# Kernel optimization log

Hardware: AMD Instinct MI355X
Metric: run time of the kernel (lower is better)

The kernel has to match this reference:

```python
import jax, jax.numpy as jnp
import numpy as np

BN_EPS = 1e-5
ITER_N = 5

def _bn(x, gamma, beta, mean, var, axis):
    shape = [1] * x.ndim
    shape[axis] = -1
    r = lambda v: v.reshape(shape)
    return (x - r(mean)) * (r(gamma) / jnp.sqrt(r(var) + BN_EPS)) + r(beta)

def _covpool(x):
    # x: (B, d, M); MPNCOV CovpoolLayer: y = x @ I_hat @ x^T, I_hat = (1/M)I - (1/M^2)11^T
    M = x.shape[-1]
    I_hat = (-1.0 / (M * M)) * jnp.ones((M, M), x.dtype) + (1.0 / M) * jnp.eye(M, dtype=x.dtype)
    return jnp.einsum('bdm,mn,ben->bde', x, I_hat, x)

def _sqrtm_ns(A, iterN=ITER_N):
    # MPNCOV SqrtmLayer: trace-normalized Newton-Schulz iteration
    d = A.shape[-1]
    I3 = 3.0 * jnp.eye(d, dtype=A.dtype)
    normA = jnp.trace(A, axis1=1, axis2=2) / 3.0          # (B,)
    A_n = A / normA[:, None, None]
    ZY = 0.5 * (I3 - A_n)
    Y = A_n @ ZY
    Z = ZY
    for _ in range(iterN - 2):
        ZY = 0.5 * (I3 - Z @ Y)
        Y = Y @ ZY
        Z = ZY @ Z
    YZY = 0.5 * (Y @ (I3 - Z @ Y))
    return YZY * jnp.sqrt(normA)[:, None, None]

def setup_inputs() -> dict:
    key = jax.random.key(0)
    ks = jax.random.split(key, 12)
    B, C, H, W = 64, 1024, 16, 16
    D, R = 128, H * W  # att_dim, sp_reso
    return {
        'x': jax.random.normal(ks[0], (B, C, H, W), jnp.float32),
        'w_dr': jax.random.normal(ks[1], (D, C), jnp.float32) * 0.02,
        'b_dr': jax.random.normal(ks[2], (D,), jnp.float32) * 0.02,
        'bn1_gamma': jnp.ones((D,), jnp.float32),
        'bn1_beta': jnp.zeros((D,), jnp.float32),
        'bn1_mean': jax.random.normal(ks[3], (D,), jnp.float32) * 0.1,
        'bn1_var': jax.random.uniform(ks[4], (D,), jnp.float32, 0.5, 1.5),
        'bn2_gamma': jnp.ones((R,), jnp.float32),
        'bn2_beta': jnp.zeros((R,), jnp.float32),
        'bn2_mean': jax.random.normal(ks[5], (R,), jnp.float32) * 0.1,
        'bn2_var': jax.random.uniform(ks[6], (R,), jnp.float32, 0.5, 1.5),
        'rc_w': jax.random.normal(ks[7], (R,), jnp.float32) * 0.1 + 1.0,
        'rc_b': jax.random.normal(ks[8], (R,), jnp.float32) * 0.02,
        'fc_w': jax.random.normal(ks[9], (R, R * R), jnp.float32) * 0.004,
        'fc_b': jax.random.normal(ks[10], (R,), jnp.float32) * 0.02,
    }

def reference(x, w_dr, b_dr, bn1_gamma, bn1_beta, bn1_mean, bn1_var,
              bn2_gamma, bn2_beta, bn2_mean, bn2_var, rc_w, rc_b, fc_w, fc_b):
    B, C, H, W = x.shape
    # 1x1 dimension-reduction conv + BN + ReLU
    y = jnp.einsum('bchw,dc->bdhw', x, w_dr) + b_dr[None, :, None, None]
    y = jax.nn.relu(_bn(y, bn1_gamma, bn1_beta, bn1_mean, bn1_var, axis=1))
    # (B, D, HW) -> (B, HW, D): HW spatial positions as 'channels', D as samples
    y = y.reshape(B, -1, H * W).transpose(0, 2, 1)
    cov = _covpool(y)                  # (B, HW, HW)
    s = _sqrtm_ns(cov, ITER_N)         # (B, HW, HW)
    # row BN over first HW axis (channels of the (B, HW, HW, 1) view)
    s = _bn(s, bn2_gamma, bn2_beta, bn2_mean, bn2_var, axis=1)
    # grouped (depthwise) 1x1 row conv: per-row scale + bias
    s = s * rc_w[None, :, None] + rc_b[None, :, None]
    att = jax.nn.sigmoid(s.reshape(B, -1) @ fc_w.T + fc_b)   # (B, HW)
    att = att.reshape(B, 1, H, W)
    return x * att
```

## Files before the change

kernel.cpp:

```cpp
#include <hip/hip_runtime.h>

typedef unsigned short u16;
typedef unsigned int   u32;
typedef __attribute__((ext_vector_type(8))) short bf8;
typedef __attribute__((ext_vector_type(4))) float f4;
typedef __attribute__((ext_vector_type(16))) float f16f;

#define MFMA(a,b,c)   __builtin_amdgcn_mfma_f32_16x16x32_bf16(a,b,c,0,0,0)
#define MFMA32(a,b,c) __builtin_amdgcn_mfma_f32_32x32x16_bf16(a,b,c,0,0,0)

__device__ __forceinline__ u16 f2bf(float f){
  u32 u = __float_as_uint(f);
  u += 0x7fffu + ((u >> 16) & 1u);
  return (u16)(u >> 16);
}
__device__ __forceinline__ float bf2f(u16 h){ return __uint_as_float(((u32)h) << 16); }
__device__ __forceinline__ u32 pk2(float a, float b){ return (u32)f2bf(a) | ((u32)f2bf(b) << 16); }

__device__ __forceinline__ void glds16(const u16* g, u16* l){
  __builtin_amdgcn_global_load_lds((const __attribute__((address_space(1))) u32*)g,
                                   (__attribute__((address_space(3))) u32*)l, 16, 0, 0);
}

__device__ __forceinline__ bf8 ldsFrag(const char* m, int row0, int k0, int pitch){
  int l = threadIdx.x & 63;
  int r = row0 + (l & 15);
  int kb = ((k0 + ((l >> 4) << 3)) << 1) ^ ((r & 7) << 4);
  return *(const bf8*)(m + r * pitch + kb);
}
__device__ __forceinline__ void ldsPut(char* m, int row, int col, int pitch, u16 v){
  int kb = (col << 1) ^ ((row & 7) << 4);
  *(u16*)(m + row * pitch + kb) = v;
}

__device__ __forceinline__ bf8 fragNS(const char* m, int r0, int ks, int l){
  int r = r0 + (l & 31);
  int kb = ((ks << 5) + ((l >> 5) << 4)) ^ ((r & 15) << 4);
  return *(const bf8*)(m + r * 256 + kb);
}
__device__ __forceinline__ bf8 fragWT(const char* m, int r0, int ks, int l){
  int r = r0 + (l & 31);
  int kb = ((ks << 5) + ((l >> 5) << 4)) ^ ((r & 15) << 4);
  return *(const bf8*)(m + r * 512 + kb);
}
__device__ __forceinline__ char* nsAddr(char* m, int row, int col4){
  return m + row * 256 + ((col4 << 1) ^ ((row & 15) << 4));
}

__device__ __forceinline__ void mmPass(const char* A, const char* B, f16f (&acc)[2][2],
                                       int R0, int C0, int l){
  #pragma unroll
  for (int ks = 0; ks < 8; ++ks){
    bf8 a0 = fragNS(A, R0,      ks, l);
    bf8 a1 = fragNS(A, R0 + 32, ks, l);
    bf8 b0 = fragNS(B, C0,      ks, l);
    bf8 b1 = fragNS(B, C0 + 32, ks, l);
    acc[0][0] = MFMA32(a0, b0, acc[0][0]); acc[0][1] = MFMA32(a0, b1, acc[0][1]);
    acc[1][0] = MFMA32(a1, b0, acc[1][0]); acc[1][1] = MFMA32(a1, b1, acc[1][1]);
  }
}

__device__ __forceinline__ void writeTile(char* D, const f16f (&acc)[2][2], int R0, int C0, int l,
                                          float scale, float dval, const uint2* adv){
  #pragma unroll
  for (int ri = 0; ri < 2; ++ri)
  #pragma unroll
  for (int ci = 0; ci < 2; ++ci)
  #pragma unroll
  for (int g = 0; g < 4; ++g){
    int srow = C0 + ci * 32 + (l & 31);
    int scol = R0 + ri * 32 + g * 8 + ((l >> 5) << 2);
    float v[4];
    #pragma unroll
    for (int q = 0; q < 4; ++q){
      float x = scale * acc[ri][ci][g * 4 + q];
      x += ((scol + q) == srow) ? dval : 0.f;
      v[q] = x;
    }
    if (adv){
      uint2 ad = adv[(ri * 2 + ci) * 4 + g];
      v[0] += 1.5f * bf2f((u16)ad.x);
      v[1] += 1.5f * bf2f((u16)(ad.x >> 16));
      v[2] += 1.5f * bf2f((u16)ad.y);
      v[3] += 1.5f * bf2f((u16)(ad.y >> 16));
    }
    *(uint2*)nsAddr(D, srow, scol) = make_uint2(pk2(v[0], v[1]), pk2(v[2], v[3]));
  }
}

__global__ __launch_bounds__(256) void k_prep(const float* __restrict__ wdr,
                                              float* __restrict__ logits,
                                              u16* __restrict__ prep){
  int i = blockIdx.x * 256 + threadIdx.x;
  if (i < 16384) logits[i] = 0.f;
  #pragma unroll
  for (int j = 0; j < 2; ++j){
    int e = i + j * 65536;
    int chunk = e >> 13, rem = e & 8191, d = rem >> 6, cb2 = rem & 63;
    int c = ((cb2 * 2) ^ ((d & 7) << 4)) >> 1;
    prep[e] = f2bf(wdr[d * 1024 + chunk * 64 + c]);
  }
}

__global__ __launch_bounds__(512) void k_conv(
    const u16* __restrict__ wprep, const float* __restrict__ x, const float* __restrict__ bdr,
    const float* __restrict__ g1, const float* __restrict__ be1,
    const float* __restrict__ m1, const float* __restrict__ v1,
    u16* __restrict__ Wg, u16* __restrict__ WTg){
  __shared__ union {
    struct { u16 A[4][8192]; u16 Bt[2][2048]; } s;
    struct { float y[128 * 33]; float musum[512]; float mu[32]; } e;
  } sm;
  int t = threadIdx.x;
  int b = blockIdx.x >> 3, hw0 = (blockIdx.x & 7) * 32;
  const float* xb = x + (size_t)b * 262144 + hw0;

  int w = t >> 6, l = t & 63;
  int d0 = (w >> 1) * 32, hh = (w & 1) * 16;
  int lc = l & 15, lr = (l >> 4) * 4;

  const f4 fz = {0.f, 0.f, 0.f, 0.f};
  f4 acc[2]; acc[0] = fz; acc[1] = fz;

  int cp = t >> 5, hwl = t & 31;
  int bo0 = (4 * cp) ^ ((hwl & 7) << 4);
  int bo1 = (4 * cp + 64) ^ ((hwl & 7) << 4);

  float br[3][4];
  #pragma unroll
  for (int j = 0; j < 3; ++j){
    glds16(wprep + j * 8192 + t * 8,        sm.s.A[j] + t * 8);
    glds16(wprep + j * 8192 + 4096 + t * 8, sm.s.A[j] + 4096 + t * 8);
    __builtin_amdgcn_sched_barrier(0);
    int c0 = j * 64;
    br[j][0] = xb[(size_t)(c0 + 2 * cp)      * 256 + hwl];
    br[j][1] = xb[(size_t)(c0 + 2 * cp + 1)  * 256 + hwl];
    br[j][2] = xb[(size_t)(c0 + 2 * cp + 32) * 256 + hwl];
    br[j][3] = xb[(size_t)(c0 + 2 * cp + 33) * 256 + hwl];
    __builtin_amdgcn_sched_barrier(0);
  }

  #pragma unroll
  for (int k = 0; k < 16; ++k){
    if (k <= 12){
      const u16* src = wprep + (k + 3) * 8192;
      glds16(src + t * 8,        sm.s.A[(k + 3) & 3] + t * 8);
      glds16(src + 4096 + t * 8, sm.s.A[(k + 3) & 3] + 4096 + t * 8);
    }
    __builtin_amdgcn_sched_barrier(0);
    if (k <= 12)      asm volatile("s_waitcnt vmcnt(14)" ::: "memory");
    else if (k == 13) asm volatile("s_waitcnt vmcnt(12)" ::: "memory");
    else if (k == 14) asm volatile("s_waitcnt vmcnt(6)" ::: "memory");
    else              asm volatile("s_waitcnt vmcnt(0)" ::: "memory");
    __builtin_amdgcn_sched_barrier(0);
    *(u32*)((char*)sm.s.Bt[k & 1] + hwl * 128 + bo0) = pk2(br[k % 3][0], br[k % 3][1]);
    *(u32*)((char*)sm.s.Bt[k & 1] + hwl * 128 + bo1) = pk2(br[k % 3][2], br[k % 3][3]);
    __builtin_amdgcn_sched_barrier(0);
    if (k <= 12){
      int c0 = (k + 3) * 64;
      br[k % 3][0] = xb[(size_t)(c0 + 2 * cp)      * 256 + hwl];
      br[k % 3][1] = xb[(size_t)(c0 + 2 * cp + 1)  * 256 + hwl];
      br[k % 3][2] = xb[(size_t)(c0 + 2 * cp + 32) * 256 + hwl];
      br[k % 3][3] = xb[(size_t)(c0 + 2 * cp + 33) * 256 + hwl];
    }
    __builtin_amdgcn_sched_barrier(0);
    asm volatile("s_waitcnt lgkmcnt(0)" ::: "memory");
    __builtin_amdgcn_sched_barrier(0);
    __builtin_amdgcn_s_barrier();
    __builtin_amdgcn_sched_barrier(0);
    #pragma unroll
    for (int ks = 0; ks < 2; ++ks){
      int k0 = ks * 32;
      bf8 a0 = ldsFrag((const char*)sm.s.A[k & 3], d0,      k0, 128);
      bf8 a1 = ldsFrag((const char*)sm.s.A[k & 3], d0 + 16, k0, 128);
      bf8 b0 = ldsFrag((const char*)sm.s.Bt[k & 1], hh, k0, 128);
      acc[0] = MFMA(a0, b0, acc[0]);
      acc[1] = MFMA(a1, b0, acc[1]);
    }
    __builtin_amdgcn_sched_barrier(0);
    __builtin_amdgcn_s_barrier();
    __builtin_amdgcn_sched_barrier(0);
  }
  __syncthreads();

  #pragma unroll
  for (int i = 0; i < 2; ++i)
    #pragma unroll
    for (int r = 0; r < 4; ++r){
      int d = d0 + i * 16 + lr + r;
      float s1 = g1[d] * rsqrtf(v1[d] + 1e-5f);
      float t1 = (bdr[d] - m1[d]) * s1 + be1[d];
      int hwp = hh + lc;
      sm.e.y[d * 33 + hwp] = fmaxf(acc[i][r] * s1 + t1, 0.f);
    }
  __syncthreads();
  { int part = t >> 5, col = t & 31;
    float s = 0.f;
    #pragma unroll
    for (int i2 = 0; i2 < 8; ++i2) s += sm.e.y[(part * 8 + i2) * 33 + col];
    sm.e.musum[part * 32 + col] = s;
  }
  __syncthreads();
  if (t < 32){
    float m = 0.f;
    #pragma unroll
    for (int p = 0; p < 16; ++p) m += sm.e.musum[p * 32 + t];
    sm.e.mu[t] = m * (1.0f / 128.0f);
  }
  __syncthreads();
  const float ISM = 0.08838834764831845f;
  { int hwp = t >> 4, dc = (t & 15) * 8;
    float muv = sm.e.mu[hwp];
    u32 q[4];
    #pragma unroll
    for (int jj = 0; jj < 4; ++jj){
      float a = (sm.e.y[(dc + 2 * jj)     * 33 + hwp] - muv) * ISM;
      float c = (sm.e.y[(dc + 2 * jj + 1) * 33 + hwp] - muv) * ISM;
      q[jj] = pk2(a, c);
    }
    *(uint4*)(Wg + ((size_t)(b * 256 + hw0 + hwp) * 128 + dc)) = make_uint4(q[0], q[1], q[2], q[3]);
  }
  { int d = t >> 2, hc = (t & 3) * 8;
    u32 q[4];
    #pragma unroll
    for (int jj = 0; jj < 4; ++jj){
      int h0 = hc + 2 * jj, h1 = hc + 2 * jj + 1;
      float a = (sm.e.y[d * 33 + h0] - sm.e.mu[h0]) * ISM;
      float c = (sm.e.y[d * 33 + h1] - sm.e.mu[h1]) * ISM;
      q[jj] = pk2(a, c);
    }
    *(uint4*)(WTg + ((size_t)(b * 128 + d) * 256 + hw0 + hc)) = make_uint4(q[0], q[1], q[2], q[3]);
  }
}

extern __shared__ char smns[];
__global__ __launch_bounds__(512, 2) void k_ns(const u16* __restrict__ WT,
                                               u16* __restrict__ yf, float* __restrict__ normAg){
  int b = blockIdx.x, t = threadIdx.x;
  char* Yb = smns;
  char* Zb = smns + 32768;
  char* T1 = smns + 65536;
  char* T2 = smns + 98304;
  char* T3 = smns + 131072;
  char* WTl = smns + 65536;
  char* G   = T3;
  float* trp = (float*)smns;

  int w = t >> 6, l = t & 63;
  int wq = w & 3;
  int R0 = (wq >> 1) * 64, C0 = (wq & 1) * 64;

  { const u16* src = WT + (size_t)b * 32768;
    int row = t >> 2, q = t & 3;
    #pragma unroll
    for (int j = 0; j < 8; ++j) {
      int c16 = q + j * 4;
      bf8 v = *(const bf8*)(src + row * 256 + c16 * 8);
      int ph = c16 ^ (row & 15);
      *(bf8*)(WTl + row * 512 + ph * 16) = v;
    }
  }
  if (t == 0) *trp = 0.f;
  __syncthreads();

  int R0g = (w & 3) * 32, C0g = (w >> 2) * 64;
  const f16f fz16 = {};
  f16f gac[2]; gac[0] = fz16; gac[1] = fz16;
  #pragma unroll
  for (int ks = 0; ks < 16; ++ks){
    bf8 a  = fragWT(WTl, R0g,      ks, l);
    bf8 b0 = fragWT(WTl, C0g,      ks, l);
    bf8 b1 = fragWT(WTl, C0g + 32, ks, l);
    gac[0] = MFMA32(a, b0, gac[0]);
    gac[1] = MFMA32(a, b1, gac[1]);
  }
  float tp = 0.f;
  #pragma unroll
  for (int ci = 0; ci < 2; ++ci)
    #pragma unroll
    for (int e = 0; e < 16; ++e){
      int row = R0g + (e & 3) + 8 * (e >> 2) + ((l >> 5) << 2);
      int col = C0g + ci * 32 + (l & 31);
      if (row == col) tp += gac[ci][e];
    }
  #pragma unroll
  for (int off = 32; off > 0; off >>= 1) tp += __shfl_down(tp, off);
  if (l == 0) atomicAdd(trp, tp);
  __syncthreads();

  float normA = fmaxf(*trp / 3.0f, 1e-12f);
  if (t == 0) normAg[b] = normA;
  float inv = 1.0f / normA;
  #pragma unroll
  for (int ci = 0; ci < 2; ++ci)
    #pragma unroll
    for (int g = 0; g < 4; ++g){
      int srow = C0g + ci * 32 + (l & 31);
      int scol = R0g + g * 8 + ((l >> 5) << 2);
      float v0 = gac[ci][g * 4 + 0] * inv, v1 = gac[ci][g * 4 + 1] * inv;
      float v2 = gac[ci][g * 4 + 2] * inv, v3 = gac[ci][g * 4 + 3] * inv;
      *(uint2*)nsAddr(G, srow, scol) = make_uint2(pk2(v0, v1), pk2(v2, v3));
    }
  __syncthreads();

  bf8 gA[8], gB[8];
  #pragma unroll
  for (int ks = 0; ks < 8; ++ks){
    gA[ks] = fragNS(G, C0,      ks, l);
    gB[ks] = fragNS(G, C0 + 32, ks, l);
  }
  { int row = t >> 2, q4 = t & 3;
    #pragma unroll
    for (int j = 0; j < 4; ++j){
      int c16 = q4 * 4 + j;
      int ph = c16 ^ (row & 15);
      bf8 gg = *(const bf8*)(G + row * 256 + ph * 16);
      bf8 yv, zv;
      #pragma unroll
      for (int e = 0; e < 8; ++e){
        int col = c16 * 8 + e;
        float y = -0.5f * bf2f((u16)gg[e]) + ((col == row) ? 1.5f : 0.f);
        yv[e] = (short)f2bf(y);
        zv[e] = (col == row) ? (short)f2bf(-0.5f) : (short)0;
      }
      *(bf8*)(Yb + row * 256 + ph * 16) = yv;
      *(bf8*)(Zb + row * 256 + ph * 16) = zv;
    }
  }
  __syncthreads();

  float z0 = 1.5f;
  for (int it = 0; it < 4; ++it){
    {
      f16f acc[2][2]; acc[0][0] = fz16; acc[0][1] = fz16; acc[1][0] = fz16; acc[1][1] = fz16;
      const char* As = (w < 4) ? Zb : Yb;
      #pragma unroll
      for (int ks = 0; ks < 8; ++ks){
        bf8 a0 = fragNS(As, R0,      ks, l);
        bf8 a1 = fragNS(As, R0 + 32, ks, l);
        acc[0][0] = MFMA32(a0, gA[ks], acc[0][0]); acc[0][1] = MFMA32(a0, gB[ks], acc[0][1]);
        acc[1][0] = MFMA32(a1, gA[ks], acc[1][0]); acc[1][1] = MFMA32(a1, gB[ks], acc[1][1]);
      }
      writeTile((w < 4) ? T1 : T3, acc, R0, C0, l, 1.0f, (w < 4) ? z0 : 0.f, nullptr);
    }
    __syncthreads();

    uint2 adv[16];
    {
      const char* addsrc = (w < 4) ? Zb : Yb;
      #pragma unroll
      for (int ri = 0; ri < 2; ++ri)
      #pragma unroll
      for (int ci = 0; ci < 2; ++ci)
      #pragma unroll
      for (int g = 0; g < 4; ++g){
        int srow = C0 + ci * 32 + (l & 31);
        int scol = R0 + ri * 32 + g * 8 + ((l >> 5) << 2);
        adv[(ri * 2 + ci) * 4 + g] = *(const uint2*)nsAddr((char*)addsrc, srow, scol);
      }
      int hC0 = C0 + ((w >> 2) << 5);
      f16f a2[2]; a2[0] = fz16; a2[1] = fz16;
      #pragma unroll
      for (int ks = 0; ks < 8; ++ks){
        bf8 a0 = fragNS(T1, R0,      ks, l);
        bf8 a1 = fragNS(T1, R0 + 32, ks, l);
        bf8 b0 = fragNS(Yb, hC0,     ks, l);
        a2[0] = MFMA32(a0, b0, a2[0]);
        a2[1] = MFMA32(a1, b0, a2[1]);
      }
      #pragma unroll
      for (int ri = 0; ri < 2; ++ri)
      #pragma unroll
      for (int g = 0; g < 4; ++g){
        int srow = hC0 + (l & 31);
        int scol = R0 + ri * 32 + g * 8 + ((l >> 5) << 2);
        float v0 = -0.5f * a2[ri][g * 4 + 0], v1 = -0.5f * a2[ri][g * 4 + 1];
        float v2 = -0.5f * a2[ri][g * 4 + 2], v3 = -0.5f * a2[ri][g * 4 + 3];
        *(uint2*)nsAddr(T2, srow, scol) = make_uint2(pk2(v0, v1), pk2(v2, v3));
      }
    }
    __syncthreads();

    if ((w >= 4) || (it < 3)){
      f16f acc[2][2]; acc[0][0] = fz16; acc[0][1] = fz16; acc[1][0] = fz16; acc[1][1] = fz16;
      const char* A3 = (w < 4) ? T2 : T3;
      const char* B3 = (w < 4) ? T1 : T2;
      mmPass(A3, B3, acc, R0, C0, l);
      writeTile((w < 4) ? Zb : Yb, acc, R0, C0, l, 1.0f, 0.f, adv);
    }
    __syncthreads();
    z0 *= 1.5f;
  }

  { int row = t >> 2, q = t & 3;
    u16* dst = yf + (size_t)b * 16384 + row * 128;
    #pragma unroll
    for (int j = 0; j < 4; ++j) {
      int c16 = q * 4 + j;
      int ph = c16 ^ (row & 15);
      *(bf8*)(dst + c16 * 8) = *(const bf8*)(Yb + row * 256 + ph * 16);
    }
  }
}

extern __shared__ char smex[];
__global__ __launch_bounds__(512) void k_expand(
    const u16* __restrict__ Wg, const u16* __restrict__ yf, const float* __restrict__ normAg,
    const float* __restrict__ g2, const float* __restrict__ be2, const float* __restrict__ m2,
    const float* __restrict__ v2, const float* __restrict__ rcw, const float* __restrict__ rcb,
    u16* __restrict__ sp){
  int blk = blockIdx.x, b = blk >> 2, iband = blk & 3;
  char* Bm = smex;
  char* Yl = smex + 65536;
  char* El = smex + 98304;
  int t = threadIdx.x;
  { const u16* src = Wg + (size_t)b * 32768;
    int row = t >> 1, q = t & 1;
    #pragma unroll
    for (int j = 0; j < 8; ++j) {
      int c16 = q + j * 2;
      bf8 v = *(const bf8*)(src + row * 128 + c16 * 8);
      int ph = c16 ^ (row & 7);
      *(bf8*)(Bm + row * 256 + ph * 16) = v;
    } }
  { const u16* src = yf + (size_t)b * 16384;
    int row = t >> 2, q = t & 3;
    #pragma unroll
    for (int j = 0; j < 4; ++j) {
      int c16 = q + j * 4;
      bf8 v = *(const bf8*)(src + row * 128 + c16 * 8);
      int ph = c16 ^ (row & 7);
      *(bf8*)(Yl + row * 256 + ph * 16) = v;
    } }
  __syncthreads();
  int w = t >> 6, l = t & 63, lc = l & 15, lr = (l >> 4) * 4;
  const f4 fz = {0.f, 0.f, 0.f, 0.f};
  { int r0 = (w >> 2) * 32, c0 = (w & 3) * 32;
    f4 acc[2][2];
    acc[0][0] = fz; acc[0][1] = fz; acc[1][0] = fz; acc[1][1] = fz;
    #pragma unroll
    for (int kk = 0; kk < 4; ++kk) {
      int k0 = kk * 32;
      bf8 a0 = ldsFrag(Bm, iband * 64 + r0,      k0, 256);
      bf8 a1 = ldsFrag(Bm, iband * 64 + r0 + 16, k0, 256);
      bf8 b0 = ldsFrag(Yl, c0,      k0, 256);
      bf8 b1 = ldsFrag(Yl, c0 + 16, k0, 256);
      acc[0][0] = MFMA(a0, b0, acc[0][0]); acc[0][1] = MFMA(a0, b1, acc[0][1]);
      acc[1][0] = MFMA(a1, b0, acc[1][0]); acc[1][1] = MFMA(a1, b1, acc[1][1]);
    }
    #pragma unroll
    for (int i = 0; i < 2; ++i)
      #pragma unroll
      for (int j = 0; j < 2; ++j)
        #pragma unroll
        for (int r = 0; r < 4; ++r)
          ldsPut(El, r0 + i * 16 + lr + r, c0 + j * 16 + lc, 256, f2bf(acc[i][j][r]));
  }
  __syncthreads();
  { float invs = rsqrtf(normAg[b]);
    int r0 = (w >> 2) * 32, c0 = (w & 3) * 64;
    f4 acc[2][4];
    #pragma unroll
    for (int i = 0; i < 2; ++i)
      #pragma unroll
      for (int j = 0; j < 4; ++j) acc[i][j] = fz;
    #pragma unroll
    for (int kk = 0; kk < 4; ++kk) {
      int k0 = kk * 32;
      bf8 a0 = ldsFrag(El, r0,      k0, 256);
      bf8 a1 = ldsFrag(El, r0 + 16, k0, 256);
      bf8 b0 = ldsFrag(Bm, c0,      k0, 256);
      bf8 b1 = ldsFrag(Bm, c0 + 16, k0, 256);
      bf8 b2 = ldsFrag(Bm, c0 + 32, k0, 256);
      bf8 b3 = ldsFrag(Bm, c0 + 48, k0, 256);
      acc[0][0] = MFMA(a0, b0, acc[0][0]); acc[0][1] = MFMA(a0, b1, acc[0][1]);
      acc[0][2] = MFMA(a0, b2, acc[0][2]); acc[0][3] = MFMA(a0, b3, acc[0][3]);
      acc[1][0] = MFMA(a1, b0, acc[1][0]); acc[1][1] = MFMA(a1, b1, acc[1][1]);
      acc[1][2] = MFMA(a1, b2, acc[1][2]); acc[1][3] = MFMA(a1, b3, acc[1][3]);
    }
    #pragma unroll
    for (int i = 0; i < 2; ++i)
      #pragma unroll
      for (int r = 0; r < 4; ++r) {
        int il = r0 + i * 16 + lr + r;
        int ig = iband * 64 + il;
        float bs = g2[ig] * rsqrtf(v2[ig] + 1e-5f);
        float al = bs * rcw[ig];
        float be = (be2[ig] - m2[ig] * bs) * rcw[ig] + rcb[ig];
        #pragma unroll
        for (int j = 0; j < 4; ++j) {
          int jg = c0 + j * 16 + lc;
          sp[(size_t)b * 65536 + ig * 256 + jg] = f2bf(acc[i][j][r] * invs * al + be);
        }
      }
  }
}

__global__ __launch_bounds__(256) void k_fc(const u16* __restrict__ sp,
                                            const float* __restrict__ fcw,
                                            float* __restrict__ partial){
  __shared__ char Bl[2][16384];
  int kc = blockIdx.x >> 2, rq = blockIdx.x & 3;
  int t = threadIdx.x, w = t >> 6, l = t & 63;
  int k0 = kc * 512, rbase = rq * 64;
  int br0 = (w & 1) * 32;
  int cr0 = (w >> 1) * 32;

  const f4 fz = {0.f, 0.f, 0.f, 0.f};
  f4 acc[2][2];
  acc[0][0] = fz; acc[0][1] = fz; acc[1][0] = fz; acc[1][1] = fz;

  float4 fbA[8], fbB[8];
  bf8 faA[8], faB[8];

  #define LOADB(S, FB) { \
    _Pragma("unroll") \
    for (int j = 0; j < 8; ++j){ \
      int fid = t + 256 * j; \
      int row = fid >> 5, c4 = fid & 31; \
      FB[j] = *(const float4*)(fcw + (size_t)(rbase + row) * 65536 + k0 + (S) * 128 + c4 * 4); \
    } }
  #define LOADA(S, FA) { \
    _Pragma("unroll") \
    for (int g = 0; g < 2; ++g) \
    _Pragma("unroll") \
    for (int ks = 0; ks < 4; ++ks) \
      FA[g * 4 + ks] = *(const bf8*)(sp + (size_t)(br0 + 16 * g + (l & 15)) * 65536 \
                                     + k0 + (S) * 128 + ks * 32 + (l >> 4) * 8); \
    }
  #define WRITEB(CUR, FB) { \
    _Pragma("unroll") \
    for (int j = 0; j < 8; ++j){ \
      int fid = t + 256 * j; \
      int row = fid >> 5, c4 = fid & 31; \
      int off = row * 256 + ((c4 * 8) ^ ((row & 7) << 4)); \
      *(uint2*)(&Bl[CUR][0] + off) = make_uint2(pk2(FB[j].x, FB[j].y), pk2(FB[j].z, FB[j].w)); \
    } }
  #define DOMFMA(CUR, FA) { \
    _Pragma("unroll") \
    for (int ks = 0; ks < 4; ++ks){ \
      bf8 b0 = ldsFrag(&Bl[CUR][0], cr0,      ks * 32, 256); \
      bf8 b1 = ldsFrag(&Bl[CUR][0], cr0 + 16, ks * 32, 256); \
      acc[0][0] = MFMA(FA[ks],     b0, acc[0][0]); \
      acc[0][1] = MFMA(FA[ks],     b1, acc[0][1]); \
      acc[1][0] = MFMA(FA[4 + ks], b0, acc[1][0]); \
      acc[1][1] = MFMA(FA[4 + ks], b1, acc[1][1]); \
    } }
  #define FENCE __builtin_amdgcn_sched_barrier(0)
  #define BARRIER { FENCE; __builtin_amdgcn_s_barrier(); FENCE; }

  LOADB(0, fbA); LOADA(0, faA);
  LOADB(1, fbB); LOADA(1, faB);

  FENCE; asm volatile("s_waitcnt vmcnt(16)" ::: "memory"); FENCE;
  WRITEB(0, fbA);
  asm volatile("s_waitcnt lgkmcnt(0)" ::: "memory");
  BARRIER;
  DOMFMA(0, faA);
  LOADB(2, fbA); LOADA(2, faA);
  BARRIER;
  FENCE; asm volatile("s_waitcnt vmcnt(16)" ::: "memory"); FENCE;
  WRITEB(1, fbB);
  asm volatile("s_waitcnt lgkmcnt(0)" ::: "memory");
  BARRIER;
  DOMFMA(1, faB);
  LOADB(3, fbB); LOADA(3, faB);
  BARRIER;
  FENCE; asm volatile("s_waitcnt vmcnt(16)" ::: "memory"); FENCE;
  WRITEB(0, fbA);
  asm volatile("s_waitcnt lgkmcnt(0)" ::: "memory");
  BARRIER;
  DOMFMA(0, faA);
  BARRIER;
  FENCE; asm volatile("s_waitcnt vmcnt(0)" ::: "memory"); FENCE;
  WRITEB(1, fbB);
  asm volatile("s_waitcnt lgkmcnt(0)" ::: "memory");
  BARRIER;
  DOMFMA(1, faB);

  #undef LOADB
  #undef LOADA
  #undef WRITEB
  #undef DOMFMA
  #undef FENCE
  #undef BARRIER

  float* pout = partial + (size_t)kc * 16384;
  #pragma unroll
  for (int g = 0; g < 2; ++g)
    #pragma unroll
    for (int j = 0; j < 2; ++j)
      #pragma unroll
      for (int q = 0; q < 4; ++q){
        int brow = br0 + g * 16 + ((l >> 4) << 2) + q;
        int rcol = rbase + cr0 + j * 16 + (l & 15);
        pout[brow * 256 + rcol] = acc[g][j][q];
      }
}

__global__ __launch_bounds__(256) void k_red(const float* __restrict__ partial,
                                             float* __restrict__ logits){
  int i = blockIdx.x * 256 + threadIdx.x;
  float s0 = 0.f, s1 = 0.f, s2 = 0.f, s3 = 0.f;
  #pragma unroll 8
  for (int kc = 0; kc < 128; kc += 4){
    s0 += partial[(size_t)(kc + 0) * 16384 + i];
    s1 += partial[(size_t)(kc + 1) * 16384 + i];
    s2 += partial[(size_t)(kc + 2) * 16384 + i];
    s3 += partial[(size_t)(kc + 3) * 16384 + i];
  }
  logits[i] = (s0 + s1) + (s2 + s3);
}

__global__ __launch_bounds__(256) void k_mul(const float* __restrict__ x,
                                             const float* __restrict__ logits,
                                             const float* __restrict__ fcb,
                                             float* __restrict__ out, int n4){
  int i = blockIdx.x * 256 + threadIdx.x;
  int str = gridDim.x * 256;
  for (; i < n4; i += str) {
    int e = i << 2;
    int b = e >> 18;
    int hw = e & 255;
    float4 xv = ((const float4*)x)[i];
    float4 lg = *(const float4*)(logits + (b << 8) + hw);
    float4 fb = *(const float4*)(fcb + hw);
    float4 o;
    o.x = xv.x / (1.f + expf(-(lg.x + fb.x)));
    o.y = xv.y / (1.f + expf(-(lg.y + fb.y)));
    o.z = xv.z / (1.f + expf(-(lg.z + fb.z)));
    o.w = xv.w / (1.f + expf(-(lg.w + fb.w)));
    ((float4*)out)[i] = o;
  }
}

extern "C" void kernel_launch(void* const* d_in, const int* in_sizes, int n_in,
                              void* d_out, int out_size, void* d_ws, size_t ws_size,
                              hipStream_t stream){
  const float* x   = (const float*)d_in[0];
  const float* wdr = (const float*)d_in[1];
  const float* bdr = (const float*)d_in[2];
  const float* g1  = (const float*)d_in[3];
  const float* be1 = (const float*)d_in[4];
  const float* m1  = (const float*)d_in[5];
  const float* v1  = (const float*)d_in[6];
  const float* g2  = (const float*)d_in[7];
  const float* be2 = (const float*)d_in[8];
  const float* m2  = (const float*)d_in[9];
  const float* v2  = (const float*)d_in[10];
  const float* rcw = (const float*)d_in[11];
  const float* rcb = (const float*)d_in[12];
  const float* fcw = (const float*)d_in[13];
  const float* fcb = (const float*)d_in[14];
  float* out = (float*)d_out;
  char* ws = (char*)d_ws;
  u16*   Wg  = (u16*)(ws);
  u16*   WTg = (u16*)(ws + (4u  << 20));
  u16*   yfg = (u16*)(ws + (8u  << 20));
  float* nAg = (float*)(ws + (10u << 20));
  u16*   wpr = (u16*)(ws + (10u << 20) + 4096);
  u16*   spg = (u16*)(ws + (11u << 20));
  float* lgt = (float*)(ws + (20u << 20));
  float* prt = (float*)(ws + (24u << 20));

  hipFuncSetAttribute((const void*)k_ns,     hipFuncAttributeMaxDynamicSharedMemorySize, 163840);
  hipFuncSetAttribute((const void*)k_expand, hipFuncAttributeMaxDynamicSharedMemorySize, 114688);

  k_prep  <<<256,  256, 0,      stream>>>(wdr, lgt, wpr);
  k_conv  <<<512,  512, 0,      stream>>>(wpr, x, bdr, g1, be1, m1, v1, Wg, WTg);
  k_ns    <<<64,   512, 163840, stream>>>(WTg, yfg, nAg);
  k_expand<<<256,  512, 114688, stream>>>(Wg, yfg, nAg, g2, be2, m2, v2, rcw, rcb, spg);
  k_fc    <<<512,  256, 0,      stream>>>(spg, fcw, prt);
  k_red   <<<64,   256, 0,      stream>>>(prt, lgt);
  k_mul   <<<2048, 256, 0,      stream>>>(x, lgt, fcb, out, 4194304);
}
```

Before: 113.9 us.

## Split FC GEMM into more K-chunks and parallelize partial-sum reduction

The FC split-K kernel now gives each block a 128-wide K slice, launched as 2048 blocks instead of 512 blocks with a 4-stage software pipeline. Each block does one load, one LDS write and one MFMA pass, relying on more blocks in flight to hide memory latency. The reduction kernel now sums 512 partials with 8 thread groups per output plus an LDS combine over 512 blocks. Partial-buffer traffic grows fourfold (32 MB written and reread), and the prt workspace region must be large enough to hold it.

```diff
diff --git a/kernel.cpp b/kernel.cpp
--- a/kernel.cpp
+++ b/kernel.cpp
@@ -499,91 +499,48 @@
 __global__ __launch_bounds__(256) void k_fc(const u16* __restrict__ sp,
                                             const float* __restrict__ fcw,
                                             float* __restrict__ partial){
-  __shared__ char Bl[2][16384];
+  __shared__ char Bl[16384];
   int kc = blockIdx.x >> 2, rq = blockIdx.x & 3;
   int t = threadIdx.x, w = t >> 6, l = t & 63;
-  int k0 = kc * 512, rbase = rq * 64;
+  int k0 = kc * 128, rbase = rq * 64;
   int br0 = (w & 1) * 32;
   int cr0 = (w >> 1) * 32;
+
+  float4 fb[8];
+  #pragma unroll
+  for (int j = 0; j < 8; ++j){
+    int fid = t + 256 * j;
+    int row = fid >> 5, c4 = fid & 31;
+    fb[j] = *(const float4*)(fcw + (size_t)(rbase + row) * 65536 + k0 + c4 * 4);
+  }
+  bf8 fa[8];
+  #pragma unroll
+  for (int g = 0; g < 2; ++g)
+    #pragma unroll
+    for (int ks = 0; ks < 4; ++ks)
+      fa[g * 4 + ks] = *(const bf8*)(sp + (size_t)(br0 + 16 * g + (l & 15)) * 65536
+                                     + k0 + ks * 32 + (l >> 4) * 8);
+  #pragma unroll
+  for (int j = 0; j < 8; ++j){
+    int fid = t + 256 * j;
+    int row = fid >> 5, c4 = fid & 31;
+    int off = row * 256 + ((c4 * 8) ^ ((row & 7) << 4));
+    *(uint2*)(Bl + off) = make_uint2(pk2(fb[j].x, fb[j].y), pk2(fb[j].z, fb[j].w));
+  }
+  __syncthreads();
 
   const f4 fz = {0.f, 0.f, 0.f, 0.f};
   f4 acc[2][2];
   acc[0][0] = fz; acc[0][1] = fz; acc[1][0] = fz; acc[1][1] = fz;
-
-  float4 fbA[8], fbB[8];
-  bf8 faA[8], faB[8];
-
-  #define LOADB(S, FB) { \
-    _Pragma("unroll") \
-    for (int j = 0; j < 8; ++j){ \
-      int fid = t + 256 * j; \
-      int row = fid >> 5, c4 = fid & 31; \
-      FB[j] = *(const float4*)(fcw + (size_t)(rbase + row) * 65536 + k0 + (S) * 128 + c4 * 4); \
-    } }
-  #define LOADA(S, FA) { \
-    _Pragma("unroll") \
-    for (int g = 0; g < 2; ++g) \
-    _Pragma("unroll") \
-    for (int ks = 0; ks < 4; ++ks) \
-      FA[g * 4 + ks] = *(const bf8*)(sp + (size_t)(br0 + 16 * g + (l & 15)) * 65536 \
-                                     + k0 + (S) * 128 + ks * 32 + (l >> 4) * 8); \
-    }
-  #define WRITEB(CUR, FB) { \
-    _Pragma("unroll") \
-    for (int j = 0; j < 8; ++j){ \
-      int fid = t + 256 * j; \
-      int row = fid >> 5, c4 = fid & 31; \
-      int off = row * 256 + ((c4 * 8) ^ ((row & 7) << 4)); \
-      *(uint2*)(&Bl[CUR][0] + off) = make_uint2(pk2(FB[j].x, FB[j].y), pk2(FB[j].z, FB[j].w)); \
-    } }
-  #define DOMFMA(CUR, FA) { \
-    _Pragma("unroll") \
-    for (int ks = 0; ks < 4; ++ks){ \
-      bf8 b0 = ldsFrag(&Bl[CUR][0], cr0,      ks * 32, 256); \
-      bf8 b1 = ldsFrag(&Bl[CUR][0], cr0 + 16, ks * 32, 256); \
-      acc[0][0] = MFMA(FA[ks],     b0, acc[0][0]); \
-      acc[0][1] = MFMA(FA[ks],     b1, acc[0][1]); \
-      acc[1][0] = MFMA(FA[4 + ks], b0, acc[1][0]); \
-      acc[1][1] = MFMA(FA[4 + ks], b1, acc[1][1]); \
-    } }
-  #define FENCE __builtin_amdgcn_sched_barrier(0)
-  #define BARRIER { FENCE; __builtin_amdgcn_s_barrier(); FENCE; }
-
-  LOADB(0, fbA); LOADA(0, faA);
-  LOADB(1, fbB); LOADA(1, faB);
-
-  FENCE; asm volatile("s_waitcnt vmcnt(16)" ::: "memory"); FENCE;
-  WRITEB(0, fbA);
-  asm volatile("s_waitcnt lgkmcnt(0)" ::: "memory");
-  BARRIER;
-  DOMFMA(0, faA);
-  LOADB(2, fbA); LOADA(2, faA);
-  BARRIER;
-  FENCE; asm volatile("s_waitcnt vmcnt(16)" ::: "memory"); FENCE;
-  WRITEB(1, fbB);
-  asm volatile("s_waitcnt lgkmcnt(0)" ::: "memory");
-  BARRIER;
-  DOMFMA(1, faB);
-  LOADB(3, fbB); LOADA(3, faB);
-  BARRIER;
-  FENCE; asm volatile("s_waitcnt vmcnt(16)" ::: "memory"); FENCE;
-  WRITEB(0, fbA);
-  asm volatile("s_waitcnt lgkmcnt(0)" ::: "memory");
-  BARRIER;
-  DOMFMA(0, faA);
-  BARRIER;
-  FENCE; asm volatile("s_waitcnt vmcnt(0)" ::: "memory"); FENCE;
-  WRITEB(1, fbB);
-  asm volatile("s_waitcnt lgkmcnt(0)" ::: "memory");
-  BARRIER;
-  DOMFMA(1, faB);
-
-  #undef LOADB
-  #undef LOADA
-  #undef WRITEB
-  #undef DOMFMA
-  #undef FENCE
-  #undef BARRIER
+  #pragma unroll
+  for (int ks = 0; ks < 4; ++ks){
+    bf8 b0 = ldsFrag(Bl, cr0,      ks * 32, 256);
+    bf8 b1 = ldsFrag(Bl, cr0 + 16, ks * 32, 256);
+    acc[0][0] = MFMA(fa[ks],     b0, acc[0][0]);
+    acc[0][1] = MFMA(fa[ks],     b1, acc[0][1]);
+    acc[1][0] = MFMA(fa[4 + ks], b0, acc[1][0]);
+    acc[1][1] = MFMA(fa[4 + ks], b1, acc[1][1]);
+  }
 
   float* pout = partial + (size_t)kc * 16384;
   #pragma unroll
@@ -600,16 +557,24 @@
 
 __global__ __launch_bounds__(256) void k_red(const float* __restrict__ partial,
                                              float* __restrict__ logits){
-  int i = blockIdx.x * 256 + threadIdx.x;
+  __shared__ float red[256];
+  int tl = threadIdx.x & 31, s = threadIdx.x >> 5;
+  int o = blockIdx.x * 32 + tl;
   float s0 = 0.f, s1 = 0.f, s2 = 0.f, s3 = 0.f;
-  #pragma unroll 8
-  for (int kc = 0; kc < 128; kc += 4){
-    s0 += partial[(size_t)(kc + 0) * 16384 + i];
-    s1 += partial[(size_t)(kc + 1) * 16384 + i];
-    s2 += partial[(size_t)(kc + 2) * 16384 + i];
-    s3 += partial[(size_t)(kc + 3) * 16384 + i];
-  }
-  logits[i] = (s0 + s1) + (s2 + s3);
+  for (int kc = s; kc < 512; kc += 32){
+    s0 += partial[(size_t)(kc     ) * 16384 + o];
+    s1 += partial[(size_t)(kc +  8) * 16384 + o];
+    s2 += partial[(size_t)(kc + 16) * 16384 + o];
+    s3 += partial[(size_t)(kc + 24) * 16384 + o];
+  }
+  red[threadIdx.x] = (s0 + s1) + (s2 + s3);
+  __syncthreads();
+  if (threadIdx.x < 32){
+    float v = 0.f;
+    #pragma unroll
+    for (int p = 0; p < 8; ++p) v += red[p * 32 + threadIdx.x];
+    logits[o] = v;
+  }
 }
 
 __global__ __launch_bounds__(256) void k_mul(const float* __restrict__ x,
@@ -670,7 +635,7 @@
   k_conv  <<<512,  512, 0,      stream>>>(wpr, x, bdr, g1, be1, m1, v1, Wg, WTg);
   k_ns    <<<64,   512, 163840, stream>>>(WTg, yfg, nAg);
   k_expand<<<256,  512, 114688, stream>>>(Wg, yfg, nAg, g2, be2, m2, v2, rcw, rcb, spg);
-  k_fc    <<<512,  256, 0,      stream>>>(spg, fcw, prt);
-  k_red   <<<64,   256, 0,      stream>>>(prt, lgt);
+  k_fc    <<<2048, 256, 0,      stream>>>(spg, fcw, prt);
+  k_red   <<<512,  256, 0,      stream>>>(prt, lgt);
   k_mul   <<<2048, 256, 0,      stream>>>(x, lgt, fcb, out, 4194304);
 }
```

New measurement: 114.1 us. About the same (+0.2%).
